# Kernel optimization log

Measured on AMD Instinct MI355X. Metric: run time of the kernel, lower is better.

The kernel has to match this reference:

```python
import jax, jax.numpy as jnp
import numpy as np

DIM = 2048
NH = 16
NKV = 4
HD = DIM // NH            # 128
KVD = HD * NKV            # 512
MLP = int(DIM * 4.0 * 2 / 3)  # 5461
EPS = 1.1920929e-07       # torch.finfo(float32).eps (nn.RMSNorm default)
ROPE_BASE = 10000.0


def act_quant(x):
    # per-token int8 absmax quantization (BitNet b1.58)
    scale = 127.0 / jnp.clip(jnp.max(jnp.abs(x), axis=-1, keepdims=True), 1e-5)
    return jnp.clip(jnp.round(x * scale), -128.0, 127.0) / scale


def weight_quant(w):
    # ternary weights via mean-absmax scale (BitNet b1.58)
    scale = 1.0 / jnp.clip(jnp.mean(jnp.abs(w)), 1e-5)
    return jnp.clip(jnp.round(w * scale), -1.0, 1.0) / scale


def bitlinear(x, w, b=None):
    # straight-through estimator quantization, then dense matmul
    xq = x + jax.lax.stop_gradient(act_quant(x) - x)
    wq = w + jax.lax.stop_gradient(weight_quant(w) - w)
    y = xq @ wq.T
    return y if b is None else y + b


def rmsnorm(x, w):
    return x * jax.lax.rsqrt(jnp.mean(x * x, axis=-1, keepdims=True) + EPS) * w


def rope_cos_sin(pos, head_dim, dtype):
    inv_freq = 1.0 / (ROPE_BASE ** (jnp.arange(0, head_dim, 2, dtype=jnp.float32) / head_dim))
    freqs = pos[..., None].astype(jnp.float32) * inv_freq  # [B,N,HD/2]
    cos = jnp.repeat(jnp.cos(freqs), 2, axis=-1).astype(dtype)  # interleaved [B,N,HD]
    sin = jnp.repeat(jnp.sin(freqs), 2, axis=-1).astype(dtype)
    return cos, sin


def rotate_interleave(x):
    x1 = x[..., 0::2]
    x2 = x[..., 1::2]
    return jnp.stack([-x2, x1], axis=-1).reshape(x.shape)


def apply_rope(x, cos, sin):
    # x: [B,H,N,HD]; cos/sin: [B,N,HD]
    return x * cos[:, None] + rotate_interleave(x) * sin[:, None]


def setup_inputs() -> dict:
    key = jax.random.key(0)
    ks = jax.random.split(key, 16)
    B, N = 2, 2048
    s = 0.02
    return {
        "x": jax.random.normal(ks[0], (B, N, DIM), jnp.float32),
        "position_ids": jnp.broadcast_to(jnp.arange(N, dtype=jnp.int32), (B, N)),
        "norm1_w": jnp.ones((DIM,), jnp.float32),
        "q_w": jax.random.normal(ks[1], (DIM, DIM), jnp.float32) * s,
        "q_b": jnp.zeros((DIM,), jnp.float32),
        "k_w": jax.random.normal(ks[2], (KVD, DIM), jnp.float32) * s,
        "k_b": jnp.zeros((KVD,), jnp.float32),
        "v_w": jax.random.normal(ks[3], (KVD, DIM), jnp.float32) * s,
        "v_b": jnp.zeros((KVD,), jnp.float32),
        "o_w": jax.random.normal(ks[4], (DIM, DIM), jnp.float32) * s,
        "norm2_w": jnp.ones((DIM,), jnp.float32),
        "gate_w": jax.random.normal(ks[5], (MLP, DIM), jnp.float32) * s,
        "up_w": jax.random.normal(ks[6], (MLP, DIM), jnp.float32) * s,
        "down_w": jax.random.normal(ks[7], (DIM, MLP), jnp.float32) * s,
    }


def reference(x, position_ids, norm1_w, q_w, q_b, k_w, k_b, v_w, v_b, o_w,
              norm2_w, gate_w, up_w, down_w):
    B, N, C = x.shape
    # --- attention ---
    h = rmsnorm(x, norm1_w)
    q = bitlinear(h, q_w, q_b).reshape(B, N, NH, HD).transpose(0, 2, 1, 3)
    k = bitlinear(h, k_w, k_b).reshape(B, N, NKV, HD).transpose(0, 2, 1, 3)
    v = bitlinear(h, v_w, v_b).reshape(B, N, NKV, HD).transpose(0, 2, 1, 3)
    cos, sin = rope_cos_sin(position_ids, HD, x.dtype)
    q = apply_rope(q, cos, sin)
    k = apply_rope(k, cos, sin)
    g = NH // NKV
    k = jnp.repeat(k, g, axis=1)  # GQA head expansion -> [B,NH,N,HD]
    v = jnp.repeat(v, g, axis=1)
    scores = jnp.einsum('bhqd,bhkd->bhqk', q, k) * (HD ** -0.5)
    causal_mask = jnp.triu(jnp.ones((N, N), bool), 1)
    scores = jnp.where(causal_mask, -jnp.inf, scores)
    attn = jax.nn.softmax(scores, axis=-1)
    out = jnp.einsum('bhqk,bhkd->bqhd', attn, v).reshape(B, N, C)
    x = x + bitlinear(out, o_w)
    # --- SwiGLU MLP ---
    h = rmsnorm(x, norm2_w)
    x = x + bitlinear(jax.nn.silu(bitlinear(h, gate_w)) * bitlinear(h, up_w), down_w)
    return x
```

## Files before the change

### kernel.cpp

```cpp
#include <hip/hip_runtime.h>

typedef unsigned short u16;
typedef unsigned int   u32;
typedef unsigned char  u8;

using bf16x8 = __attribute__((ext_vector_type(8))) short;
using f32x4  = __attribute__((ext_vector_type(4))) float;
using i32x4  = __attribute__((ext_vector_type(4))) int;

#define SEQ    2048
#define DIMC   2048
#define TOK    4096
#define QKV_N  3072
#define GU_N   11008
#define MLP_P  5504
#define MLP_R  5461
#define ATT_SCALE 0.08838834764831845f

__device__ __forceinline__ float bf2f(u16 v){ return __uint_as_float(((u32)v) << 16); }
__device__ __forceinline__ u16 f2bf(float f){
  u32 x = __float_as_uint(f);
  u32 r = (x + 0x7fffu + ((x >> 16) & 1u)) >> 16;
  return (u16)r;
}

__device__ __forceinline__ float waveRedSum(float v){
#pragma unroll
  for (int o = 32; o > 0; o >>= 1) v += __shfl_xor(v, o);
  return v;
}
__device__ __forceinline__ float waveRedMax(float v){
#pragma unroll
  for (int o = 32; o > 0; o >>= 1) v = fmaxf(v, __shfl_xor(v, o));
  return v;
}

#define GLD16(gp, lp) __builtin_amdgcn_global_load_lds( \
    (__attribute__((address_space(1))) void*)(gp), \
    (__attribute__((address_space(3))) void*)(lp), 16, 0, 0)

#define FENCE() asm volatile("" ::: "memory")
#define SBAR()  do{ FENCE(); __builtin_amdgcn_s_barrier(); FENCE(); }while(0)
#define VMCNT(n) asm volatile("s_waitcnt vmcnt(" #n ")" ::: "memory")

__global__ __launch_bounds__(256) void k_abssum7(
    const float4* __restrict__ w0, const float4* __restrict__ w1,
    const float4* __restrict__ w2, const float4* __restrict__ w3,
    const float4* __restrict__ w4, const float4* __restrict__ w5,
    const float4* __restrict__ w6, float* __restrict__ sc){
  const int rg = blockIdx.y;
  const float4* w = rg==0?w0: rg==1?w1: rg==2?w2: rg==3?w3: rg==4?w4: rg==5?w5: w6;
  const int n4 = (rg==0||rg==3) ? 1048576 : (rg<4 ? 262144 : 2796032);
  float s = 0.f;
  for (int i = blockIdx.x*256 + threadIdx.x; i < n4; i += gridDim.x*256){
    float4 v = w[i];
    s += fabsf(v.x) + fabsf(v.y) + fabsf(v.z) + fabsf(v.w);
  }
  s = waveRedSum(s);
  __shared__ float sm[4];
  int lane = threadIdx.x & 63, wv = threadIdx.x >> 6;
  if (lane == 0) sm[wv] = s;
  __syncthreads();
  if (threadIdx.x == 0) atomicAdd(sc + rg, sm[0]+sm[1]+sm[2]+sm[3]);
}

__global__ void k_finalize(float* __restrict__ sc){
  if (threadIdx.x == 0){
    const float counts[7] = {4194304.f, 1048576.f, 1048576.f, 4194304.f,
                             11184128.f, 11184128.f, 11184128.f};
    for (int i = 0; i < 7; i++) sc[8+i] = fmaxf(sc[i]/counts[i], 1e-5f);
  }
}

__global__ __launch_bounds__(256) void k_wquant6(
    const float4* __restrict__ w0, const float4* __restrict__ w1,
    const float4* __restrict__ w2, const float4* __restrict__ w3,
    const float4* __restrict__ w4, const float4* __restrict__ w5,
    u32* __restrict__ d0, u32* __restrict__ d1, u32* __restrict__ d2,
    u32* __restrict__ d3, u32* __restrict__ d4, u32* __restrict__ d5,
    const float* __restrict__ sc){
  const int rg = blockIdx.y;
  const float4* src = rg==0?w0: rg==1?w1: rg==2?w2: rg==3?w3: rg==4?w4: w5;
  u32* dst = rg==0?d0: rg==1?d1: rg==2?d2: rg==3?d3: rg==4?d4: d5;
  const int n4 = (rg==0||rg==3) ? 1048576 : (rg<4 ? 262144 : 2796032);
  float ws = 1.0f / sc[8+rg];
  for (int i = blockIdx.x*256 + threadIdx.x; i < n4; i += gridDim.x*256){
    float4 v = src[i];
    int c0 = (int)fminf(fmaxf(rintf(v.x*ws), -1.f), 1.f);
    int c1 = (int)fminf(fmaxf(rintf(v.y*ws), -1.f), 1.f);
    int c2 = (int)fminf(fmaxf(rintf(v.z*ws), -1.f), 1.f);
    int c3 = (int)fminf(fmaxf(rintf(v.w*ws), -1.f), 1.f);
    dst[i] = (u32)(u8)c0 | ((u32)(u8)c1 << 8) | ((u32)(u8)c2 << 16) | ((u32)(u8)c3 << 24);
  }
}

__global__ __launch_bounds__(256) void k_wquant_down(const float* __restrict__ src,
                                                     u32* __restrict__ dst,
                                                     const float* __restrict__ deqp){
  int i = blockIdx.x*256 + threadIdx.x;
  const int total = 2048*(MLP_P/4);
  if (i >= total) return;
  float ws = 1.0f / deqp[0];
  int r = i / (MLP_P/4);
  int c4 = (i - r*(MLP_P/4))*4;
  u32 o = 0;
#pragma unroll
  for (int e = 0; e < 4; e++){
    int c = c4 + e;
    int t = 0;
    if (c < MLP_R) t = (int)fminf(fmaxf(rintf(src[(long)r*MLP_R + c]*ws), -1.f), 1.f);
    o |= (u32)(u8)t << (8*e);
  }
  dst[i] = o;
}

__global__ __launch_bounds__(256) void k_rmsq(const float* __restrict__ in,
                                              const float* __restrict__ nw,
                                              char* __restrict__ outq,
                                              float* __restrict__ rowdeq, int do_norm){
  const int row = blockIdx.x, tid = threadIdx.x;
  const float* xp = in + (long)row * DIMC + tid*8;
  float v[8];
  float4 a0 = *(const float4*)xp;
  float4 a1 = *(const float4*)(xp + 4);
  v[0]=a0.x; v[1]=a0.y; v[2]=a0.z; v[3]=a0.w;
  v[4]=a1.x; v[5]=a1.y; v[6]=a1.z; v[7]=a1.w;
  float ss = 0.f;
#pragma unroll
  for (int j = 0; j < 8; j++) ss += v[j]*v[j];
  __shared__ float sm[8];
  int lane = tid & 63, wv = tid >> 6;
  ss = waveRedSum(ss);
  if (lane == 0) sm[wv] = ss;
  __syncthreads();
  float h[8];
  float amax = 0.f;
  if (do_norm){
    float tot = sm[0]+sm[1]+sm[2]+sm[3];
    float rms = rsqrtf(tot * (1.0f/DIMC) + 1.1920929e-07f);
    float4 w0 = *(const float4*)(nw + tid*8);
    float4 w1 = *(const float4*)(nw + tid*8 + 4);
    float wr8[8] = {w0.x,w0.y,w0.z,w0.w,w1.x,w1.y,w1.z,w1.w};
#pragma unroll
    for (int j = 0; j < 8; j++){ h[j] = v[j]*rms*wr8[j]; amax = fmaxf(amax, fabsf(h[j])); }
  } else {
#pragma unroll
    for (int j = 0; j < 8; j++){ h[j] = v[j]; amax = fmaxf(amax, fabsf(h[j])); }
  }
  amax = waveRedMax(amax);
  if (lane == 0) sm[4+wv] = amax;
  __syncthreads();
  float gmax = fmaxf(fmaxf(sm[4],sm[5]), fmaxf(sm[6],sm[7]));
  float sc = 127.0f / fmaxf(gmax, 1e-5f);
  int2 o;
  char* oc = (char*)&o;
#pragma unroll
  for (int j = 0; j < 8; j++)
    oc[j] = (char)(int)fminf(fmaxf(rintf(h[j]*sc), -128.f), 127.f);
  *(int2*)(outq + (long)row*DIMC + tid*8) = o;
  if (tid == 0) rowdeq[row] = 1.0f / sc;
}

__global__ __launch_bounds__(256) void k_ropevt2(u16* __restrict__ y,
                                                 const int* __restrict__ pos_ids,
                                                 u16* __restrict__ VT){
  if (blockIdx.x < 4096){
    const int m = blockIdx.x, tid = threadIdx.x;
    __shared__ float cs[64], sn[64];
    if (tid < 64){
      float pos = (float)pos_ids[m];
      float inv = expf((float)tid * -0.14391156831212787f);
      float s, c;
      sincosf(pos * inv, &s, &c);
      cs[tid] = c; sn[tid] = s;
    }
    __syncthreads();
    u32* row = (u32*)(y + (long)m*QKV_N);
#pragma unroll
    for (int it = 0; it < 5; it++){
      int p = it*256 + tid;
      int i = p & 63;
      u32 both = row[p];
      float x0 = bf2f((u16)(both & 0xffffu));
      float x1 = bf2f((u16)(both >> 16));
      float c = cs[i], s = sn[i];
      u16 o0 = f2bf(x0*c - x1*s);
      u16 o1 = f2bf(x1*c + x0*s);
      row[p] = (u32)o0 | ((u32)o1 << 16);
    }
  } else {
    int idx = (int)(blockIdx.x - 4096)*256 + threadIdx.x;
    int d  = idx & 127;
    int hk = (idx >> 7) & 3;
    int b  = (idx >> 9) & 1;
    int tg = idx >> 10;
    int tok0 = tg*8;
    const u16* src = y + ((long)b*SEQ + tok0)*QKV_N + 2560 + hk*128 + d;
    u16 tmp[8];
#pragma unroll
    for (int e = 0; e < 8; e++) tmp[e] = src[(long)e*QKV_N];
    *(int4*)(VT + (((long)(b*4+hk))*128 + d)*SEQ + tok0) = *(int4*)tmp;
  }
}

template<int BM, int BN, int WM, int WN, int MODE>
__global__ __launch_bounds__(512, 2) void k_gemm8(
    const char* __restrict__ A, const char* __restrict__ B,
    int K, int lda, int ldb, int ldc, int ntn,
    const float* __restrict__ rowdeq, const float* __restrict__ deqp,
    const float* __restrict__ bq, const float* __restrict__ bk, const float* __restrict__ bv,
    const float* __restrict__ resid, float* __restrict__ outF, u16* __restrict__ outB)
{
  constexpr int SM = BM/WM, SN = BN/WN;
  constexpr int MR = SM/16, NR = SN/16, MRH = MR/2;
  constexpr int RA = BM/128, RB = BN/128;
  constexpr int ASZ = BM*64, BSZ = BN*64;
  constexpr int BUFSZ = 2*(ASZ+BSZ);
  extern __shared__ __align__(16) char sm8[];

  const int tid = threadIdx.x;
  const int lane = tid & 63, wv = tid >> 6;
  const int wr = wv / WN, wc = wv % WN;
  const int r = lane & 15, qq = lane >> 4;

  const int nwg = gridDim.x;
  const int chunk = nwg >> 3;
  const int lin = blockIdx.x;
  const int swz = (lin & 7)*chunk + (lin >> 3);
  const int mt = swz / ntn, nt = swz - mt*ntn;
  const long m0 = (long)mt*BM, n0 = (long)nt*BN;

  const char* __restrict__ gA = A + m0*lda;
  const char* __restrict__ gB = B + n0*ldb;

  int  soA[RA], soB[RB];
  long goA[RA], goB[RB];
#pragma unroll
  for (int u = 0; u < RA; u++){
    int c = u*512 + tid, row = c >> 2, gp = c & 3, g = gp ^ ((row>>1)&3);
    soA[u] = c*16; goA[u] = (long)row*lda + g*16;
  }
#pragma unroll
  for (int u = 0; u < RB; u++){
    int c = u*512 + tid, row = c >> 2, gp = c & 3, g = gp ^ ((row>>1)&3);
    soB[u] = c*16; goB[u] = (long)row*ldb + g*16;
  }
  const int gsw = (qq ^ ((r>>1)&3))*16;
  const int aoff0 = (wr*SM + r)*64 + gsw;
  const int boff0 = (wc*SN + r)*64 + gsw;

  const int NT = K >> 7;

  i32x4 acc[MR][NR];
#pragma unroll
  for (int i = 0; i < MR; i++)
#pragma unroll
    for (int j = 0; j < NR; j++) acc[i][j] = (i32x4){0,0,0,0};

  auto stA = [&](int tq, int kh){
    char* dst = sm8 + (tq&1)*BUFSZ + kh*ASZ;
    const char* src = gA + (long)tq*128 + kh*64;
#pragma unroll
    for (int u = 0; u < RA; u++) GLD16(src + goA[u], dst + soA[u]);
  };
  auto stB = [&](int tq, int kh){
    char* dst = sm8 + (tq&1)*BUFSZ + 2*ASZ + kh*BSZ;
    const char* src = gB + (long)tq*128 + kh*64;
#pragma unroll
    for (int u = 0; u < RB; u++) GLD16(src + goB[u], dst + soB[u]);
  };

  stA(0,0); stB(0,0); stA(0,1); stB(0,1);
  stA(1,0); stB(1,0);
  if constexpr (RA+RB == 4) VMCNT(4); else VMCNT(3);
  SBAR();

  for (int t = 0; t < NT; t++){
    const char* cA = sm8 + (t&1)*BUFSZ;
    const char* cB = cA + 2*ASZ;
    i32x4 bF[NR];
    {
      i32x4 aF[MRH];
#pragma unroll
      for (int i = 0; i < MRH; i++) aF[i] = *(const i32x4*)(cA + aoff0 + i*1024);
#pragma unroll
      for (int j = 0; j < NR; j++)  bF[j] = *(const i32x4*)(cB + boff0 + j*1024);
      if (t+1 < NT) stA(t+1, 1);
      SBAR();
      __builtin_amdgcn_s_setprio(1);
#pragma unroll
      for (int i = 0; i < MRH; i++)
#pragma unroll
        for (int j = 0; j < NR; j++)
          acc[i][j] = __builtin_amdgcn_mfma_i32_16x16x64_i8(aF[i], bF[j], acc[i][j], 0,0,0);
      __builtin_amdgcn_s_setprio(0);
      SBAR();
    }
    {
      i32x4 aF[MRH];
#pragma unroll
      for (int i = 0; i < MRH; i++) aF[i] = *(const i32x4*)(cA + aoff0 + (MRH+i)*1024);
      if (t+1 < NT) stB(t+1, 1);
      SBAR();
      __builtin_amdgcn_s_setprio(1);
#pragma unroll
      for (int i = 0; i < MRH; i++)
#pragma unroll
        for (int j = 0; j < NR; j++)
          acc[MRH+i][j] = __builtin_amdgcn_mfma_i32_16x16x64_i8(aF[i], bF[j], acc[MRH+i][j], 0,0,0);
      __builtin_amdgcn_s_setprio(0);
      SBAR();
    }
    {
      i32x4 aF[MRH];
#pragma unroll
      for (int i = 0; i < MRH; i++) aF[i] = *(const i32x4*)(cA + ASZ + aoff0 + i*1024);
#pragma unroll
      for (int j = 0; j < NR; j++)  bF[j] = *(const i32x4*)(cB + BSZ + boff0 + j*1024);
      if (t+2 < NT) stA(t+2, 0);
      SBAR();
      __builtin_amdgcn_s_setprio(1);
#pragma unroll
      for (int i = 0; i < MRH; i++)
#pragma unroll
        for (int j = 0; j < NR; j++)
          acc[i][j] = __builtin_amdgcn_mfma_i32_16x16x64_i8(aF[i], bF[j], acc[i][j], 0,0,0);
      __builtin_amdgcn_s_setprio(0);
      SBAR();
    }
    {
      i32x4 aF[MRH];
#pragma unroll
      for (int i = 0; i < MRH; i++) aF[i] = *(const i32x4*)(cA + ASZ + aoff0 + (MRH+i)*1024);
      if (t+2 < NT) stB(t+2, 0);
      SBAR();
      __builtin_amdgcn_s_setprio(1);
#pragma unroll
      for (int i = 0; i < MRH; i++)
#pragma unroll
        for (int j = 0; j < NR; j++)
          acc[MRH+i][j] = __builtin_amdgcn_mfma_i32_16x16x64_i8(aF[i], bF[j], acc[MRH+i][j], 0,0,0);
      __builtin_amdgcn_s_setprio(0);
      if (t + 1 < NT){
        if (t + 2 < NT){ if constexpr (RA+RB == 4) VMCNT(4); else VMCNT(3); }
        else VMCNT(0);
      }
      SBAR();
    }
  }

#pragma unroll
  for (int i = 0; i < MR; i++){
#pragma unroll
    for (int tt = 0; tt < 4; tt++){
      const long row = m0 + wr*SM + 16*i + 4*qq + tt;
      const float rdv = rowdeq[row];
#pragma unroll
      for (int j = 0; j < NR; j++){
        const long col = n0 + wc*SN + 16*j + r;
        float vv = (float)acc[i][j][tt];
        if constexpr (MODE == 0){
          int sec = (col >= 2048) + (col >= 2560);
          float dq = deqp[sec];
          float bias = (sec == 0) ? bq[col] : (sec == 1) ? bk[col-2048] : bv[col-2560];
          outB[row*(long)ldc + col] = f2bf(vv*rdv*dq + bias);
        } else if constexpr (MODE == 1){
          outF[row*(long)ldc + col] = vv*rdv*deqp[0] + resid[row*(long)ldc + col];
        } else {
          int sec = (col >= 5504) ? 1 : 0;
          outB[row*(long)ldc + col] = f2bf(vv*rdv*deqp[sec]);
        }
      }
    }
  }
}

__global__ __launch_bounds__(256) void k_attn(const u16* __restrict__ Y,
                                              const u16* __restrict__ VT,
                                              float* __restrict__ O)
{
  __shared__ u16 Ks[64*128];
  __shared__ u16 VTs[128*64];
  __shared__ u16 Ps[64][72];

  const int pp = blockIdx.x;
  const int bh = blockIdx.y;
  const int b = bh >> 4, h = bh & 15, hk = h >> 2;
  const int tid = threadIdx.x;
  const int lane = tid & 63, wv = tid >> 6;
  const int r = lane & 15, qq = lane >> 4;
  const long rowbase = (long)b * SEQ;
  const u16* Kbase = Y + rowbase*QKV_N + 2048 + hk*128;
  const u16* Vbase = VT + ((long)(b*4+hk))*128*SEQ;

  for (int ph = 0; ph < 2; ph++){
    const int qt = ph ? pp : 31 - pp;
    const int q0 = qt * 64;

    bf16x8 qf[4];
#pragma unroll
    for (int kc = 0; kc < 4; kc++)
      qf[kc] = *(const bf16x8*)(Y + (rowbase + q0 + wv*16 + r)*QKV_N + h*128 + kc*32 + qq*8);

#pragma unroll
    for (int rnd = 0; rnd < 4; rnd++){
      int c = rnd*256 + tid;
      int row = c >> 4, g = (c & 15) ^ (row & 7);
      GLD16(Kbase + ((long)(qt*0 + row))*QKV_N + g*8, (char*)Ks + c*16);
    }
#pragma unroll
    for (int rnd = 0; rnd < 4; rnd++){
      int c = rnd*256 + tid;
      int d = c >> 3, g = (c & 7) ^ (d & 7);
      GLD16(Vbase + (long)d*SEQ + g*8, (char*)VTs + c*16);
    }
    __syncthreads();

    f32x4 accO[8];
#pragma unroll
    for (int jn = 0; jn < 8; jn++) accO[jn] = (f32x4){0.f,0.f,0.f,0.f};
    float m_run[4] = {-INFINITY,-INFINITY,-INFINITY,-INFINITY};
    float l_run[4] = {0.f,0.f,0.f,0.f};

    for (int kt = 0; kt <= qt; kt++){
      float sv[4][4];
#pragma unroll
      for (int j = 0; j < 4; j++){
        f32x4 a = (f32x4){0.f,0.f,0.f,0.f};
#pragma unroll
        for (int kc = 0; kc < 4; kc++){
          bf16x8 kf = *(const bf16x8*)(Ks + (16*j + r)*128 + (((kc*4 + qq) ^ (r & 7)))*8);
          a = __builtin_amdgcn_mfma_f32_16x16x32_bf16(qf[kc], kf, a, 0, 0, 0);
        }
#pragma unroll
        for (int t = 0; t < 4; t++) sv[j][t] = a[t] * ATT_SCALE;
      }
      __syncthreads();
      if (kt < qt){
#pragma unroll
        for (int rnd = 0; rnd < 4; rnd++){
          int c = rnd*256 + tid;
          int row = c >> 4, g = (c & 15) ^ (row & 7);
          GLD16(Kbase + ((long)((kt+1)*64 + row))*QKV_N + g*8, (char*)Ks + c*16);
        }
      }
      if (kt == qt){
#pragma unroll
        for (int j = 0; j < 4; j++){
          int key = kt*64 + 16*j + r;
#pragma unroll
          for (int t = 0; t < 4; t++){
            int qr = q0 + wv*16 + 4*qq + t;
            if (key > qr) sv[j][t] = -INFINITY;
          }
        }
      }
#pragma unroll
      for (int t = 0; t < 4; t++){
        float mm = fmaxf(fmaxf(sv[0][t],sv[1][t]), fmaxf(sv[2][t],sv[3][t]));
#pragma unroll
        for (int o = 8; o > 0; o >>= 1) mm = fmaxf(mm, __shfl_xor(mm, o));
        float mnew = fmaxf(m_run[t], mm);
        float alpha = __expf(m_run[t] - mnew);
        m_run[t] = mnew;
        float ps = 0.f;
#pragma unroll
        for (int j = 0; j < 4; j++){
          float p = __expf(sv[j][t] - mnew);
          ps += p;
          Ps[wv*16 + 4*qq + t][16*j + r] = f2bf(p);
        }
#pragma unroll
        for (int o = 8; o > 0; o >>= 1) ps += __shfl_xor(ps, o);
        l_run[t] = l_run[t]*alpha + ps;
#pragma unroll
        for (int jn = 0; jn < 8; jn++) accO[jn][t] *= alpha;
      }
#pragma unroll
      for (int kc = 0; kc < 2; kc++){
        bf16x8 pf = *(const bf16x8*)&Ps[wv*16 + r][kc*32 + qq*8];
#pragma unroll
        for (int jn = 0; jn < 8; jn++){
          bf16x8 vf = *(const bf16x8*)(VTs + (16*jn + r)*64 + (((kc*4 + qq) ^ (r & 7)))*8);
          accO[jn] = __builtin_amdgcn_mfma_f32_16x16x32_bf16(pf, vf, accO[jn], 0, 0, 0);
        }
      }
      __syncthreads();
      if (kt < qt){
#pragma unroll
        for (int rnd = 0; rnd < 4; rnd++){
          int c = rnd*256 + tid;
          int d = c >> 3, g = (c & 7) ^ (d & 7);
          GLD16(Vbase + (long)d*SEQ + (kt+1)*64 + g*8, (char*)VTs + c*16);
        }
      }
    }
    float inv[4];
#pragma unroll
    for (int t = 0; t < 4; t++) inv[t] = 1.0f / l_run[t];
#pragma unroll
    for (int jn = 0; jn < 8; jn++){
#pragma unroll
      for (int t = 0; t < 4; t++){
        long row = rowbase + q0 + wv*16 + 4*qq + t;
        O[row*DIMC + h*128 + 16*jn + r] = accO[jn][t]*inv[t];
      }
    }
    __syncthreads();
  }
}

__global__ __launch_bounds__(256) void k_swiglu(const u16* __restrict__ ygu,
                                                char* __restrict__ qout,
                                                float* __restrict__ rowdeq){
  const int row = blockIdx.x, tid = threadIdx.x;
  const u16* base = ygu + (long)row * GU_N;
  float h[24];
  float amax = 0.f;
#pragma unroll
  for (int it = 0; it < 3; it++){
    int chunk = it*256 + tid;
    if (chunk < 688){
      int j0 = chunk*8;
      int4 g4 = *(const int4*)(base + j0);
      int4 u4 = *(const int4*)(base + MLP_P + j0);
      const u16* gp = (const u16*)&g4;
      const u16* up = (const u16*)&u4;
#pragma unroll
      for (int e = 0; e < 8; e++){
        float g = bf2f(gp[e]);
        float u = bf2f(up[e]);
        float hv = g * (1.0f/(1.0f + __expf(-g))) * u;
        h[it*8+e] = hv;
        amax = fmaxf(amax, fabsf(hv));
      }
    } else {
#pragma unroll
      for (int e = 0; e < 8; e++) h[it*8+e] = 0.f;
    }
  }
  amax = waveRedMax(amax);
  __shared__ float sm[4];
  int lane = tid & 63, wv = tid >> 6;
  if (lane == 0) sm[wv] = amax;
  __syncthreads();
  float gmax = fmaxf(fmaxf(sm[0],sm[1]), fmaxf(sm[2],sm[3]));
  float sc = 127.0f / fmaxf(gmax, 1e-5f);
#pragma unroll
  for (int it = 0; it < 3; it++){
    int chunk = it*256 + tid;
    if (chunk < 688){
      int j0 = chunk*8;
      int2 o;
      char* oc = (char*)&o;
#pragma unroll
      for (int e = 0; e < 8; e++)
        oc[e] = (char)(int)fminf(fmaxf(rintf(h[it*8+e]*sc), -128.f), 127.f);
      *(int2*)(qout + (long)row*MLP_P + j0) = o;
    }
  }
  if (tid == 0) rowdeq[row] = 1.0f/sc;
}

extern "C" void kernel_launch(void* const* d_in, const int* in_sizes, int n_in,
                              void* d_out, int out_size, void* d_ws, size_t ws_size,
                              hipStream_t stream)
{
  (void)in_sizes; (void)n_in; (void)out_size; (void)ws_size;
  const float* x   = (const float*)d_in[0];
  const int*   pos = (const int*)d_in[1];
  const float* n1w = (const float*)d_in[2];
  const float* qw  = (const float*)d_in[3];
  const float* qb  = (const float*)d_in[4];
  const float* kw  = (const float*)d_in[5];
  const float* kb  = (const float*)d_in[6];
  const float* vw  = (const float*)d_in[7];
  const float* vb  = (const float*)d_in[8];
  const float* ow  = (const float*)d_in[9];
  const float* n2w = (const float*)d_in[10];
  const float* gw  = (const float*)d_in[11];
  const float* uw  = (const float*)d_in[12];
  const float* dw  = (const float*)d_in[13];
  float* out = (float*)d_out;
  char* ws = (char*)d_ws;

  static int attr_done = 0;
  if (!attr_done){
    hipFuncSetAttribute(reinterpret_cast<const void*>(k_gemm8<256,128,4,2,0>),
                        hipFuncAttributeMaxDynamicSharedMemorySize, 98304);
    hipFuncSetAttribute(reinterpret_cast<const void*>(k_gemm8<256,128,4,2,1>),
                        hipFuncAttributeMaxDynamicSharedMemorySize, 98304);
    hipFuncSetAttribute(reinterpret_cast<const void*>(k_gemm8<256,256,2,4,2>),
                        hipFuncAttributeMaxDynamicSharedMemorySize, 131072);
    attr_done = 1;
  }

  float* sc   = (float*)ws;
  char* Wqkv  = ws + 256;
  char* Wo    = ws + 6291712;
  char* Wgu   = ws + 10486016;
  char* Wd    = ws + 33030400;
  char* actq  = ws + 44302592;
  char* swq   = ws + 52691200;
  float* rd   = (float*)(ws + 75235584);
  char* xreg  = ws + 75252224;
  u16* yqkv   = (u16*)xreg;
  float* attn = (float*)(xreg + 25165824);
  u16* vT     = (u16*)(xreg + 58720256);
  u16* ygu    = (u16*)xreg;

  hipMemsetAsync(sc, 0, 64, stream);
  k_abssum7<<<dim3(512,7),256,0,stream>>>((const float4*)qw, (const float4*)kw,
                                          (const float4*)vw, (const float4*)ow,
                                          (const float4*)gw, (const float4*)uw,
                                          (const float4*)dw, sc);
  k_finalize<<<1,64,0,stream>>>(sc);
  k_wquant6<<<dim3(512,6),256,0,stream>>>((const float4*)qw, (const float4*)kw,
                                          (const float4*)vw, (const float4*)ow,
                                          (const float4*)gw, (const float4*)uw,
                                          (u32*)Wqkv, (u32*)(Wqkv + 2048l*2048),
                                          (u32*)(Wqkv + 2560l*2048), (u32*)Wo,
                                          (u32*)Wgu, (u32*)(Wgu + 5504l*2048), sc);
  hipMemsetAsync(Wgu + 5461l*2048,        0, 43l*2048, stream);
  hipMemsetAsync(Wgu + (5504l+5461)*2048, 0, 43l*2048, stream);
  k_wquant_down<<<11008,256,0,stream>>>(dw, (u32*)Wd, sc+14);

  k_rmsq<<<4096,256,0,stream>>>(x, n1w, actq, rd, 1);
  k_gemm8<256,128,4,2,0><<<384,512,98304,stream>>>(actq, Wqkv, 2048, 2048, 2048, 3072, 24,
                                          rd, sc+8, qb, kb, vb, nullptr, nullptr, yqkv);
  k_ropevt2<<<5120,256,0,stream>>>(yqkv, pos, vT);
  k_attn<<<dim3(16,32),256,0,stream>>>(yqkv, vT, attn);
  k_rmsq<<<4096,256,0,stream>>>(attn, n1w, actq, rd, 0);
  k_gemm8<256,128,4,2,1><<<256,512,98304,stream>>>(actq, Wo, 2048, 2048, 2048, 2048, 16,
                                          rd, sc+11, nullptr, nullptr, nullptr, x, out, nullptr);

  k_rmsq<<<4096,256,0,stream>>>(out, n2w, actq, rd, 1);
  k_gemm8<256,256,2,4,2><<<688,512,131072,stream>>>(actq, Wgu, 2048, 2048, 2048, 11008, 43,
                                          rd, sc+12, nullptr, nullptr, nullptr, nullptr, nullptr, ygu);
  k_swiglu<<<4096,256,0,stream>>>(ygu, swq, rd);
  k_gemm8<256,128,4,2,1><<<256,512,98304,stream>>>(swq, Wd, 5504, 5504, 5504, 2048, 16,
                                          rd, sc+14, nullptr, nullptr, nullptr, out, out, nullptr);
}
```

Before: 677.0 us.

## Fuse SiLU-gating into gate/up GEMM epilogue via interleaved weight layout

```diff
diff --git a/kernel.cpp b/kernel.cpp
--- a/kernel.cpp
+++ b/kernel.cpp
@@ -77,11 +77,10 @@
     const float4* __restrict__ w2, const float4* __restrict__ w3,
     const float4* __restrict__ w4, const float4* __restrict__ w5,
     u32* __restrict__ d0, u32* __restrict__ d1, u32* __restrict__ d2,
-    u32* __restrict__ d3, u32* __restrict__ d4, u32* __restrict__ d5,
+    u32* __restrict__ d3, u32* __restrict__ dgu,
     const float* __restrict__ sc){
   const int rg = blockIdx.y;
   const float4* src = rg==0?w0: rg==1?w1: rg==2?w2: rg==3?w3: rg==4?w4: w5;
-  u32* dst = rg==0?d0: rg==1?d1: rg==2?d2: rg==3?d3: rg==4?d4: d5;
   const int n4 = (rg==0||rg==3) ? 1048576 : (rg<4 ? 262144 : 2796032);
   float ws = 1.0f / sc[8+rg];
   for (int i = blockIdx.x*256 + threadIdx.x; i < n4; i += gridDim.x*256){
@@ -90,7 +89,15 @@
     int c1 = (int)fminf(fmaxf(rintf(v.y*ws), -1.f), 1.f);
     int c2 = (int)fminf(fmaxf(rintf(v.z*ws), -1.f), 1.f);
     int c3 = (int)fminf(fmaxf(rintf(v.w*ws), -1.f), 1.f);
-    dst[i] = (u32)(u8)c0 | ((u32)(u8)c1 << 8) | ((u32)(u8)c2 << 16) | ((u32)(u8)c3 << 24);
+    u32 pk = (u32)(u8)c0 | ((u32)(u8)c1 << 8) | ((u32)(u8)c2 << 16) | ((u32)(u8)c3 << 24);
+    if (rg < 4){
+      u32* dst = rg==0?d0: rg==1?d1: rg==2?d2: d3;
+      dst[i] = pk;
+    } else {
+      int row = i >> 9, col = i & 511;
+      int rI = 32*(row>>4) + (row&15) + ((rg==5)?16:0);
+      dgu[(long)rI*512 + col] = pk;
+    }
   }
 }
 
@@ -364,12 +371,140 @@
           float dq = deqp[sec];
           float bias = (sec == 0) ? bq[col] : (sec == 1) ? bk[col-2048] : bv[col-2560];
           outB[row*(long)ldc + col] = f2bf(vv*rdv*dq + bias);
-        } else if constexpr (MODE == 1){
+        } else {
           outF[row*(long)ldc + col] = vv*rdv*deqp[0] + resid[row*(long)ldc + col];
-        } else {
-          int sec = (col >= 5504) ? 1 : 0;
-          outB[row*(long)ldc + col] = f2bf(vv*rdv*deqp[sec]);
         }
+      }
+    }
+  }
+}
+
+template<int MODE>
+__global__ __launch_bounds__(256, 2) void k_gemm2b(
+    const char* __restrict__ A, const char* __restrict__ B,
+    int K, int lda, int ldb, int ldc, int ntn,
+    const float* __restrict__ rowdeq, const float* __restrict__ deqp,
+    u16* __restrict__ outB)
+{
+  constexpr int BM = 256, BN = 128;
+  constexpr int MR = 8, NR = 4, MRH = 4;
+  constexpr int RA = 4, RB = 2;
+  constexpr int ASZ = BM*64, BSZ = BN*64;
+  constexpr int BUFSZ = ASZ + BSZ;
+  __shared__ __align__(16) char sm8[2*BUFSZ];
+
+  const int tid = threadIdx.x;
+  const int lane = tid & 63, wv = tid >> 6;
+  const int wr = wv >> 1, wc = wv & 1;
+  const int r = lane & 15, qq = lane >> 4;
+
+  const int nwg = gridDim.x;
+  const int chunk = nwg >> 3;
+  const int lin = blockIdx.x;
+  const int swz = (lin & 7)*chunk + (lin >> 3);
+  const int mt = swz / ntn, nt = swz - mt*ntn;
+  const long m0 = (long)mt*BM, n0 = (long)nt*BN;
+
+  const char* __restrict__ gA = A + m0*lda;
+  const char* __restrict__ gB = B + n0*ldb;
+
+  int  soA[RA], soB[RB];
+  long goA[RA], goB[RB];
+#pragma unroll
+  for (int u = 0; u < RA; u++){
+    int c = u*256 + tid, row = c >> 2, g = (c & 3) ^ ((row>>1)&3);
+    soA[u] = c*16; goA[u] = (long)row*lda + g*16;
+  }
+#pragma unroll
+  for (int u = 0; u < RB; u++){
+    int c = u*256 + tid, row = c >> 2, g = (c & 3) ^ ((row>>1)&3);
+    soB[u] = c*16; goB[u] = (long)row*ldb + g*16;
+  }
+  const int gsw = (qq ^ ((r>>1)&3))*16;
+  const int aoff0 = (wr*128 + r)*64 + gsw;
+  const int boff0 = (wc*64 + r)*64 + gsw;
+
+  const int NT = K >> 6;
+
+  i32x4 acc[MR][NR];
+#pragma unroll
+  for (int i = 0; i < MR; i++)
+#pragma unroll
+    for (int j = 0; j < NR; j++) acc[i][j] = (i32x4){0,0,0,0};
+
+  auto stA = [&](int tq){
+    char* dst = sm8 + (tq&1)*BUFSZ;
+    const char* src = gA + (long)tq*64;
+#pragma unroll
+    for (int u = 0; u < RA; u++) GLD16(src + goA[u], dst + soA[u]);
+  };
+  auto stB = [&](int tq){
+    char* dst = sm8 + (tq&1)*BUFSZ + ASZ;
+    const char* src = gB + (long)tq*64;
+#pragma unroll
+    for (int u = 0; u < RB; u++) GLD16(src + goB[u], dst + soB[u]);
+  };
+
+  stA(0); stB(0); stB(1);
+  VMCNT(2);
+  SBAR();
+
+  for (int t = 0; t < NT; t++){
+    const char* cA = sm8 + (t&1)*BUFSZ;
+    const char* cB = cA + ASZ;
+    i32x4 bF[NR];
+    {
+      i32x4 aF[MRH];
+#pragma unroll
+      for (int i = 0; i < MRH; i++) aF[i] = *(const i32x4*)(cA + aoff0 + i*1024);
+#pragma unroll
+      for (int j = 0; j < NR; j++)  bF[j] = *(const i32x4*)(cB + boff0 + j*1024);
+      if (t+1 < NT) stA(t+1);
+      SBAR();
+      __builtin_amdgcn_s_setprio(1);
+#pragma unroll
+      for (int i = 0; i < MRH; i++)
+#pragma unroll
+        for (int j = 0; j < NR; j++)
+          acc[i][j] = __builtin_amdgcn_mfma_i32_16x16x64_i8(aF[i], bF[j], acc[i][j], 0,0,0);
+      __builtin_amdgcn_s_setprio(0);
+      SBAR();
+    }
+    {
+      i32x4 aF[MRH];
+#pragma unroll
+      for (int i = 0; i < MRH; i++) aF[i] = *(const i32x4*)(cA + aoff0 + (MRH+i)*1024);
+      if (t+2 < NT) stB(t+2);
+      SBAR();
+      __builtin_amdgcn_s_setprio(1);
+#pragma unroll
+      for (int i = 0; i < MRH; i++)
+#pragma unroll
+        for (int j = 0; j < NR; j++)
+          acc[MRH+i][j] = __builtin_amdgcn_mfma_i32_16x16x64_i8(aF[i], bF[j], acc[MRH+i][j], 0,0,0);
+      __builtin_amdgcn_s_setprio(0);
+      if (t + 1 < NT){
+        if (t + 2 < NT) VMCNT(2); else VMCNT(0);
+      }
+      SBAR();
+    }
+  }
+
+  const float dqg = deqp[0], dqu = deqp[1];
+#pragma unroll
+  for (int i = 0; i < MR; i++){
+#pragma unroll
+    for (int tt = 0; tt < 4; tt++){
+      const long row = m0 + wr*128 + 16*i + 4*qq + tt;
+      const float rdv = rowdeq[row];
+#pragma unroll
+      for (int j = 0; j < NR; j += 2){
+        const long col = n0 + wc*64 + 16*j + r;
+        float g = (float)acc[i][j][tt]   * rdv * dqg;
+        float u = (float)acc[i][j+1][tt] * rdv * dqu;
+        float hv = g * (1.0f/(1.0f + __expf(-g))) * u;
+        const long hcol = (col >> 5)*16 + (col & 15);
+        outB[row*(long)ldc + hcol] = f2bf(hv);
       }
     }
   }
@@ -510,11 +645,11 @@
   }
 }
 
-__global__ __launch_bounds__(256) void k_swiglu(const u16* __restrict__ ygu,
+__global__ __launch_bounds__(256) void k_hquant(const u16* __restrict__ hbuf,
                                                 char* __restrict__ qout,
                                                 float* __restrict__ rowdeq){
   const int row = blockIdx.x, tid = threadIdx.x;
-  const u16* base = ygu + (long)row * GU_N;
+  const u16* base = hbuf + (long)row * MLP_P;
   float h[24];
   float amax = 0.f;
 #pragma unroll
@@ -522,15 +657,11 @@
     int chunk = it*256 + tid;
     if (chunk < 688){
       int j0 = chunk*8;
-      int4 g4 = *(const int4*)(base + j0);
-      int4 u4 = *(const int4*)(base + MLP_P + j0);
-      const u16* gp = (const u16*)&g4;
-      const u16* up = (const u16*)&u4;
+      int4 h4 = *(const int4*)(base + j0);
+      const u16* hp = (const u16*)&h4;
 #pragma unroll
       for (int e = 0; e < 8; e++){
-        float g = bf2f(gp[e]);
-        float u = bf2f(up[e]);
-        float hv = g * (1.0f/(1.0f + __expf(-g))) * u;
+        float hv = bf2f(hp[e]);
         h[it*8+e] = hv;
         amax = fmaxf(amax, fabsf(hv));
       }
@@ -590,8 +721,6 @@
                         hipFuncAttributeMaxDynamicSharedMemorySize, 98304);
     hipFuncSetAttribute(reinterpret_cast<const void*>(k_gemm8<256,128,4,2,1>),
                         hipFuncAttributeMaxDynamicSharedMemorySize, 98304);
-    hipFuncSetAttribute(reinterpret_cast<const void*>(k_gemm8<256,256,2,4,2>),
-                        hipFuncAttributeMaxDynamicSharedMemorySize, 131072);
     attr_done = 1;
   }
 
@@ -607,9 +736,10 @@
   u16* yqkv   = (u16*)xreg;
   float* attn = (float*)(xreg + 25165824);
   u16* vT     = (u16*)(xreg + 58720256);
-  u16* ygu    = (u16*)xreg;
+  u16* hbuf   = (u16*)xreg;
 
   hipMemsetAsync(sc, 0, 64, stream);
+  hipMemsetAsync(Wgu, 0, 11008l*2048, stream);
   k_abssum7<<<dim3(512,7),256,0,stream>>>((const float4*)qw, (const float4*)kw,
                                           (const float4*)vw, (const float4*)ow,
                                           (const float4*)gw, (const float4*)uw,
@@ -620,9 +750,7 @@
                                           (const float4*)gw, (const float4*)uw,
                                           (u32*)Wqkv, (u32*)(Wqkv + 2048l*2048),
                                           (u32*)(Wqkv + 2560l*2048), (u32*)Wo,
-                                          (u32*)Wgu, (u32*)(Wgu + 5504l*2048), sc);
-  hipMemsetAsync(Wgu + 5461l*2048,        0, 43l*2048, stream);
-  hipMemsetAsync(Wgu + (5504l+5461)*2048, 0, 43l*2048, stream);
+                                          (u32*)Wgu, sc);
   k_wquant_down<<<11008,256,0,stream>>>(dw, (u32*)Wd, sc+14);
 
   k_rmsq<<<4096,256,0,stream>>>(x, n1w, actq, rd, 1);
@@ -635,9 +763,9 @@
                                           rd, sc+11, nullptr, nullptr, nullptr, x, out, nullptr);
 
   k_rmsq<<<4096,256,0,stream>>>(out, n2w, actq, rd, 1);
-  k_gemm8<256,256,2,4,2><<<688,512,131072,stream>>>(actq, Wgu, 2048, 2048, 2048, 11008, 43,
-                                          rd, sc+12, nullptr, nullptr, nullptr, nullptr, nullptr, ygu);
-  k_swiglu<<<4096,256,0,stream>>>(ygu, swq, rd);
+  k_gemm2b<3><<<1376,256,0,stream>>>(actq, Wgu, 2048, 2048, 2048, MLP_P, 86,
+                                     rd, sc+12, hbuf);
+  k_hquant<<<4096,256,0,stream>>>(hbuf, swq, rd);
   k_gemm8<256,128,4,2,1><<<256,512,98304,stream>>>(swq, Wd, 5504, 5504, 5504, 2048, 16,
                                           rd, sc+14, nullptr, nullptr, nullptr, out, out, nullptr);
 }
```

Result: no change. 670.2 us (-1.0%).
